# Kernel optimization log

Hardware: AMD Instinct MI355X
Metric: run time of the kernel (lower is better)

The kernel has to match this reference:

```python
import jax, jax.numpy as jnp
import numpy as np

D_MODEL = 1024
QK_DIM = 1024
V_DIM = 1024
H = 16
TAU = 20.0
HQK = QK_DIM // H
HV = V_DIM // H
SCALE = HQK ** -0.5
SCALE_BASE = 512.0
EPS_GAMMA = 1e-8
EPS_GN = 1e-5


def _rotate_every_two(x):
    x1 = x[..., ::2]
    x2 = x[..., 1::2]
    return jnp.stack([-x2, x1], axis=-1).reshape(x.shape)


def _xpos_rotate(q, k, t):
    # q,k: (B,H,N,d); t: (B,N) continuous positions (timestamps in days)
    d = q.shape[-1]
    inv_freq = (1.0 / (10000.0 ** (np.arange(0, d, 2) / d))).astype(np.float32)  # (d/2,)
    sinusoid = t[:, None, :, None] * inv_freq  # (B,1,N,d/2)
    sin = jnp.repeat(jnp.sin(sinusoid), 2, axis=-1)  # (B,1,N,d)
    cos = jnp.repeat(jnp.cos(sinusoid), 2, axis=-1)
    scale_vec = ((np.arange(0, d, 2) + 0.4 * d) / (1.4 * d)).astype(np.float32)  # (d/2,)
    scale = jnp.repeat(scale_vec ** (t[:, None, :, None] / SCALE_BASE), 2, axis=-1)  # (B,1,N,d)
    q_rot = (q * cos + _rotate_every_two(q) * sin) * scale
    k_rot = (k * cos + _rotate_every_two(k) * sin) / scale
    return q_rot, k_rot


def setup_inputs() -> dict:
    key = jax.random.key(0)
    ks = jax.random.split(key, 6)
    B, N = 4, 1024
    X = jax.random.normal(ks[0], (B, N, D_MODEL), dtype=jnp.float32)
    # increasing timestamps in days
    timestamps = jnp.sort(jax.random.uniform(ks[1], (B, N), jnp.float32, 0.0, 100.0), axis=-1)
    W_qkv = jax.random.normal(ks[2], (D_MODEL, 2 * QK_DIM + V_DIM), dtype=jnp.float32) * 0.02
    W_gamma = jax.random.normal(ks[3], (D_MODEL, H), dtype=jnp.float32) * 0.02
    W_gated = jax.random.normal(ks[4], (D_MODEL, V_DIM), dtype=jnp.float32) * 0.02
    W_out = jax.random.normal(ks[5], (V_DIM, D_MODEL), dtype=jnp.float32) * 0.02
    return {"X": X, "timestamps": timestamps, "W_qkv": W_qkv, "W_gamma": W_gamma,
            "W_gated": W_gated, "W_out": W_out}


def reference(X, timestamps, W_qkv, W_gamma, W_gated, W_out):
    B, N, _ = X.shape
    qkv = X @ W_qkv  # (B,N,2*qk+v)
    q, k, v = jnp.split(qkv, [QK_DIM, 2 * QK_DIM], axis=-1)
    q = q.reshape(B, N, H, HQK).transpose(0, 2, 1, 3)  # (B,H,N,dk)
    k = k.reshape(B, N, H, HQK).transpose(0, 2, 1, 3)
    v = v.reshape(B, N, H, HV).transpose(0, 2, 1, 3)
    q, k = _xpos_rotate(q, k, timestamps)
    # data-dependent decay gamma in (0,1]
    gamma = jax.nn.sigmoid(X @ W_gamma) ** (1.0 / TAU)  # (B,N,H)
    log_b = jnp.cumsum(jnp.log(gamma + EPS_GAMMA), axis=1).transpose(0, 2, 1)  # (B,H,N)
    log_D = log_b[..., :, None] - log_b[..., None, :]  # (B,H,N,N)
    causal = jnp.tril(jnp.ones((N, N), dtype=bool))
    # masked_fill(-inf) then clamp[-80,0]: clip maps -inf -> -80 (matches torch)
    D = jnp.exp(jnp.clip(jnp.where(causal, log_D, -jnp.inf), -80.0, 0.0))
    attn = jnp.einsum('bhnd,bhmd->bhnm', q, k) * SCALE * D
    O = jnp.einsum('bhnm,bhmd->bhnd', attn, v)  # (B,H,N,dv)
    O = O.transpose(0, 2, 1, 3).reshape(B, N, V_DIM)
    # GroupNorm(num_groups=H, affine=False) over (channels-in-group, seq)
    g = O.reshape(B, N, H, HV)
    mu = g.mean(axis=(1, 3), keepdims=True)
    var = g.var(axis=(1, 3), keepdims=True)
    O = ((g - mu) / jnp.sqrt(var + EPS_GN)).reshape(B, N, V_DIM)
    O = jax.nn.silu(X @ W_gated) * O
    return O @ W_out
```

## Files before the change

kernel.cpp:

```cpp
#include <hip/hip_runtime.h>
#include <cstddef>
#include <cstdint>

#define NH 16
#define HD 64
#define NSEQ 1024
#define NB 4
#define DM 1024
#define SCALE 0.125f

typedef __attribute__((ext_vector_type(8))) short v8s;
typedef __attribute__((ext_vector_type(4))) float v4f;

__device__ __forceinline__ short f2bf(float x) {
    union { float f; unsigned u; } v; v.f = x;
    unsigned r = v.u + 0x7FFF + ((v.u >> 16) & 1);
    return (short)(r >> 16);
}
__device__ __forceinline__ float bf2f(short x) {
    union { unsigned u; float f; } v; v.u = ((unsigned)(unsigned short)x) << 16;
    return v.f;
}
__device__ __forceinline__ void gload16(const void* g, void* l) {
    __builtin_amdgcn_global_load_lds(
        (const __attribute__((address_space(1))) void*)g,
        (__attribute__((address_space(3))) void*)l, 16, 0, 0);
}
__device__ __forceinline__ int gswz(int r, int kbyte) {
    return (r * 64 + kbyte) ^ (((r >> 1) & 3) << 4);
}
__device__ __forceinline__ int aswz(int r, int byte) {
    return (r * 128 + byte) ^ ((r & 7) << 4);
}
#define SBAR() __builtin_amdgcn_s_barrier()
#define WAITV0() asm volatile("s_waitcnt vmcnt(0)" ::: "memory")
#define WAITV4() asm volatile("s_waitcnt vmcnt(4)" ::: "memory")
#define WAITL() asm volatile("s_waitcnt lgkmcnt(0)" ::: "memory")

__global__ __launch_bounds__(256) void tconv3(const float* __restrict__ Wq,
                                              const float* __restrict__ Wgt,
                                              const float* __restrict__ Wo,
                                              short* __restrict__ Wtq,
                                              short* __restrict__ Wtg,
                                              short* __restrict__ Wto) {
    __shared__ short lsm[32][136];
    int ct = blockIdx.x;
    const int kt = blockIdx.y;
    const float* W; short* Bt; int N;
    if (ct < 24)      { W = Wq;  Bt = Wtq; N = 3072; }
    else if (ct < 32) { W = Wgt; Bt = Wtg; N = 1024; ct -= 24; }
    else              { W = Wo;  Bt = Wto; N = 1024; ct -= 32; }
    const int t = threadIdx.x;
    {
        const int kk = t >> 3, nn0 = (t & 7) * 16;
        const float* src = W + (size_t)(kt * 32 + kk) * N + ct * 128 + nn0;
#pragma unroll
        for (int j = 0; j < 16; j += 4) {
            float4 v = *(const float4*)(src + j);
            lsm[kk][nn0 + j] = f2bf(v.x); lsm[kk][nn0 + j + 1] = f2bf(v.y);
            lsm[kk][nn0 + j + 2] = f2bf(v.z); lsm[kk][nn0 + j + 3] = f2bf(v.w);
        }
    }
    __syncthreads();
    const int rloc = t >> 1, kb0 = (t & 1) * 16;
    short o[16] __attribute__((aligned(16)));
#pragma unroll
    for (int j = 0; j < 16; ++j) o[j] = lsm[kb0 + j][rloc];
    char* base = (char*)(Bt + ((size_t)ct * 32 + kt) * 4096);
#pragma unroll
    for (int c = 0; c < 2; ++c)
        *(v8s*)(base + gswz(rloc, kb0 * 2 + c * 16)) = *(v8s*)&o[c * 8];
}

template<int MODE>
__global__ __launch_bounds__(256) void gemm_tt(const short* __restrict__ A,
                                               const short* __restrict__ B,
                                               void* __restrict__ C, int N,
                                               const short* __restrict__ O,
                                               const float* __restrict__ partial) {
    __shared__ short As[4096];
    __shared__ short Bs[4096];
    const int tid = threadIdx.x;
    const int w = tid >> 6, l = tid & 63;
    const int wr = w >> 1, wc = w & 1;
    const int rt = blockIdx.y, ct = blockIdx.x;
    const char* Abase = (const char*)A + ((size_t)rt * 32) * 8192;
    const char* Bbase = (const char*)B + ((size_t)ct * 32) * 8192;

    v4f acc[4][4];
#pragma unroll
    for (int i = 0; i < 4; ++i)
#pragma unroll
        for (int j = 0; j < 4; ++j) acc[i][j] = (v4f){0.f, 0.f, 0.f, 0.f};

    for (int kt = 0; kt < 32; ++kt) {
        __syncthreads();
#pragma unroll
        for (int i = 0; i < 2; ++i) {
            const int c = w * 2 + i;
            gload16(Abase + (size_t)kt * 8192 + c * 1024 + l * 16, (char*)As + c * 1024);
            gload16(Bbase + (size_t)kt * 8192 + c * 1024 + l * 16, (char*)Bs + c * 1024);
        }
        __syncthreads();
        v8s af[4], bfr[4];
#pragma unroll
        for (int i = 0; i < 4; ++i) {
            const int ra = wr * 64 + i * 16 + (l & 15);
            af[i] = *(const v8s*)((char*)As + gswz(ra, (l >> 4) * 16));
            const int rb = wc * 64 + i * 16 + (l & 15);
            bfr[i] = *(const v8s*)((char*)Bs + gswz(rb, (l >> 4) * 16));
        }
#pragma unroll
        for (int i = 0; i < 4; ++i)
#pragma unroll
            for (int j = 0; j < 4; ++j)
                acc[i][j] = __builtin_amdgcn_mfma_f32_16x16x32_bf16(af[i], bfr[j], acc[i][j], 0, 0, 0);
    }
    float mu = 0.f, rstd = 0.f;
    if (MODE == 2) {
        const int hh = ct * 2 + wc;
        const int bh = (rt >> 3) * NH + hh;
        float s = 0.f, q = 0.f;
#pragma unroll
        for (int i = 0; i < 8; ++i) {
            s += partial[(bh * 8 + i) * 2];
            q += partial[(bh * 8 + i) * 2 + 1];
        }
        const float inv = 1.0f / (NSEQ * HD);
        mu = s * inv;
        rstd = rsqrtf(q * inv - mu * mu + 1e-5f);
    }
#pragma unroll
    for (int i = 0; i < 4; ++i)
#pragma unroll
        for (int j = 0; j < 4; ++j) {
            const int r0 = rt * 128 + wr * 64 + i * 16 + (l >> 4) * 4;
            const int cc = ct * 128 + wc * 64 + j * 16 + (l & 15);
#pragma unroll
            for (int t2 = 0; t2 < 4; ++t2) {
                if (MODE == 1) ((short*)C)[(size_t)(r0 + t2) * N + cc] = f2bf(acc[i][j][t2]);
                else if (MODE == 0) ((float*)C)[(size_t)(r0 + t2) * N + cc] = acc[i][j][t2];
                else {
                    const int row = r0 + t2;
                    const float g = acc[i][j][t2];
                    const float silu = g / (1.0f + __expf(-g));
                    const float ov = bf2f(O[(size_t)row * DM + cc]);
                    const float val = silu * (ov - mu) * rstd;
                    const int rloc = row - rt * 128;
                    char* base = (char*)((short*)C + ((size_t)rt * 32 + (cc >> 5)) * 4096);
                    *(short*)(base + gswz(rloc, (cc & 31) * 2)) = f2bf(val);
                }
            }
        }
}

__global__ __launch_bounds__(256) void gamma_conv(const float* __restrict__ X,
                                                  const float* __restrict__ Wg,
                                                  float* __restrict__ loggam,
                                                  short* __restrict__ Xb) {
    __shared__ float wgs[1024 * 17];
    const int tid = threadIdx.x;
#pragma unroll
    for (int it = 0; it < 16; ++it) {
        const int idx = it * 1024 + tid * 4;
        float4 v = *(const float4*)(Wg + idx);
        const int k = idx >> 4, h0 = idx & 15;
        wgs[k * 17 + h0]     = v.x;
        wgs[k * 17 + h0 + 1] = v.y;
        wgs[k * 17 + h0 + 2] = v.z;
        wgs[k * 17 + h0 + 3] = v.w;
    }
    __syncthreads();

    const int r = tid >> 4, c = tid & 15;
    const int row = blockIdx.x * 16 + r;
    const int rt = row >> 7, rloc = row & 127;
    char* xtile = (char*)(Xb + (size_t)rt * 32 * 4096);
    const float* xrow = X + (size_t)row * DM;
    float acc[16];
#pragma unroll
    for (int h = 0; h < 16; ++h) acc[h] = 0.0f;
#pragma unroll 4
    for (int i = 0; i < 16; ++i) {
        const int kb = i * 64 + c * 4;
        float4 xv = *(const float4*)(xrow + kb);
        short4 o4 = make_short4(f2bf(xv.x), f2bf(xv.y), f2bf(xv.z), f2bf(xv.w));
        *(short4*)(xtile + (size_t)(kb >> 5) * 8192 + gswz(rloc, (kb & 31) * 2)) = o4;
        const float xs[4] = {xv.x, xv.y, xv.z, xv.w};
#pragma unroll
        for (int j = 0; j < 4; ++j) {
            const float* wrow = &wgs[(kb + j) * 17];
#pragma unroll
            for (int h = 0; h < 16; ++h) acc[h] = fmaf(xs[j], wrow[h], acc[h]);
        }
    }
#pragma unroll
    for (int h = 0; h < 16; ++h) {
#pragma unroll
        for (int off = 8; off >= 1; off >>= 1)
            acc[h] += __shfl_xor(acc[h], off, 16);
    }
    const float d = acc[c];
    const float sig = 1.0f / (1.0f + expf(-d));
    const float gam = powf(sig, 1.0f / 20.0f);
    loggam[(size_t)row * NH + c] = logf(gam + 1e-8f);
}

__global__ __launch_bounds__(256) void scan_kernel(const float* __restrict__ lg,
                                                   float* __restrict__ lgT) {
    const int wave = threadIdx.x >> 6;
    const int lane = threadIdx.x & 63;
    const int bh = blockIdx.x * 4 + wave;
    const int b = bh >> 4, h = bh & 15;
    const float* p = lg + (size_t)b * NSEQ * NH + h;
    const int n0 = lane * 16;
    float v[16];
    float s = 0.0f;
#pragma unroll
    for (int j = 0; j < 16; ++j) { v[j] = p[(size_t)(n0 + j) * NH]; s += v[j]; }
    float sc = s;
#pragma unroll
    for (int off = 1; off < 64; off <<= 1) {
        float o = __shfl_up(sc, off, 64);
        if (lane >= off) sc += o;
    }
    float acc = sc - s;
    float* q = lgT + (size_t)bh * NSEQ + n0;
#pragma unroll
    for (int j = 0; j < 16; ++j) { acc += v[j]; q[j] = acc; }
}

__global__ __launch_bounds__(256) void prep(const short* __restrict__ qkvb,
                                            const float* __restrict__ ts,
                                            short* __restrict__ Qb,
                                            short* __restrict__ Kb,
                                            short* __restrict__ Vtb) {
    __shared__ short vsm[64][72];
    const int tile = blockIdx.x, bh = blockIdx.y;
    const int b = bh >> 4, h = bh & 15;
    const int t = threadIdx.x;
    const int rloc = t >> 2, d0 = (t & 3) * 16;
    const int row = b * NSEQ + tile * 64 + rloc;
    const short* src = qkvb + (size_t)row * 3072 + h * HD;
    const size_t tb = ((size_t)bh * 16 + tile) * 4096;

    float qa[16], ka[16];
    {
        v8s q0 = *(const v8s*)(src + d0), q1 = *(const v8s*)(src + d0 + 8);
        v8s k0 = *(const v8s*)(src + 1024 + d0), k1 = *(const v8s*)(src + 1024 + d0 + 8);
#pragma unroll
        for (int j = 0; j < 8; ++j) {
            qa[j] = bf2f(q0[j]); qa[j + 8] = bf2f(q1[j]);
            ka[j] = bf2f(k0[j]); ka[j + 8] = bf2f(k1[j]);
        }
    }
    const float tv = ts[row];
    short qo[16] __attribute__((aligned(16)));
    short ko[16] __attribute__((aligned(16)));
#pragma unroll
    for (int j = 0; j < 8; ++j) {
        const int i = (d0 >> 1) + j;
        const float inv_freq = exp2f(-0.4152410119f * (float)i);
        const float ang = tv * inv_freq;
        const float s = sinf(ang), c = cosf(ang);
        const float sv = ((float)(2 * i) + 25.6f) * (1.0f / 89.6f);
        const float e = log2f(sv) * tv * (1.0f / 512.0f);
        const float sc = exp2f(e) * SCALE, isc = exp2f(-e);
        qo[2 * j]     = f2bf((qa[2 * j] * c - qa[2 * j + 1] * s) * sc);
        qo[2 * j + 1] = f2bf((qa[2 * j + 1] * c + qa[2 * j] * s) * sc);
        ko[2 * j]     = f2bf((ka[2 * j] * c - ka[2 * j + 1] * s) * isc);
        ko[2 * j + 1] = f2bf((ka[2 * j + 1] * c + ka[2 * j] * s) * isc);
    }
#pragma unroll
    for (int c = 0; c < 2; ++c) {
        *(v8s*)((char*)(Qb + tb) + aswz(rloc, d0 * 2 + c * 16)) = *(v8s*)&qo[c * 8];
        *(v8s*)((char*)(Kb + tb) + aswz(rloc, d0 * 2 + c * 16)) = *(v8s*)&ko[c * 8];
    }
    {
        v8s v0 = *(const v8s*)(src + 2048 + d0), v1 = *(const v8s*)(src + 2048 + d0 + 8);
        *(short4*)&vsm[rloc][d0]      = *(short4*)&v0;
        *(short4*)&vsm[rloc][d0 + 4]  = *((short4*)&v0 + 1);
        *(short4*)&vsm[rloc][d0 + 8]  = *(short4*)&v1;
        *(short4*)&vsm[rloc][d0 + 12] = *((short4*)&v1 + 1);
    }
    __syncthreads();
    {
        const int d = t >> 2, m0 = (t & 3) * 16;
        short vt[16] __attribute__((aligned(16)));
#pragma unroll
        for (int j = 0; j < 16; ++j) vt[j] = vsm[m0 + j][d];
#pragma unroll
        for (int c = 0; c < 2; ++c)
            *(v8s*)((char*)(Vtb + tb) + aswz(d, m0 * 2 + c * 16)) = *(v8s*)&vt[c * 8];
    }
}

__global__ __launch_bounds__(256) void attn6(const short* __restrict__ Qb,
                                             const short* __restrict__ Kb,
                                             const short* __restrict__ Vtb,
                                             const float* __restrict__ logbT,
                                             short* __restrict__ O,
                                             float* __restrict__ partial) {
    __shared__ short Ks[2][4096];
    __shared__ short Vts[2][4096];
    __shared__ short Ps[8192];
    __shared__ float lbAll[1024];
    __shared__ float emAll[1024];
    const int id = blockIdx.x;
    const int half = id >> 8;
    const int idx = id & 255;
    const int bh = ((idx & 7) << 3) | ((idx >> 3) & 7);
    const int qq = half == 0 ? (4 + (idx >> 6)) : (3 - (idx >> 6));
    const int b = bh >> 4, h = bh & 15;
    const int tid = threadIdx.x;
    const int w = tid >> 6, l = tid & 63;
    const int n0 = qq * 128;
    const int NT = 2 * qq + 2;

#pragma unroll
    for (int i = 0; i < 4; ++i) {
        const int c = w * 4 + i;
        gload16((const char*)Qb + ((size_t)bh * 16 + 2 * qq) * 8192 + c * 1024 + l * 16,
                (char*)Ps + c * 1024);
    }
    for (int i = tid; i < 1024; i += 256)
        lbAll[i] = logbT[(size_t)bh * NSEQ + i];
    WAITV0(); WAITL();
    SBAR();

    const float base = lbAll[n0];
    for (int i = tid; i < NT * 64; i += 256) emAll[i] = __expf(base - lbAll[i]);
    float en[2];
#pragma unroll
    for (int rg = 0; rg < 2; ++rg)
        en[rg] = __expf(lbAll[n0 + w * 32 + rg * 16 + (l & 15)] - base);
    v8s aq[2][2];
#pragma unroll
    for (int rg = 0; rg < 2; ++rg)
#pragma unroll
        for (int kc = 0; kc < 2; ++kc) {
            const int r = w * 32 + rg * 16 + (l & 15);
            aq[rg][kc] = *(const v8s*)((char*)Ps + (r >> 6) * 8192 +
                                       aswz(r & 63, kc * 64 + (l >> 4) * 16));
        }
    WAITL();
    SBAR();

    v4f oacc[2][4];
#pragma unroll
    for (int rg = 0; rg < 2; ++rg)
#pragma unroll
        for (int dt = 0; dt < 4; ++dt) oacc[rg][dt] = (v4f){0.f, 0.f, 0.f, 0.f};

#pragma unroll
    for (int i = 0; i < 2; ++i) {
        const int c = w * 2 + i;
        gload16((const char*)Kb + ((size_t)bh * 16 + 0) * 8192 + c * 1024 + l * 16,
                (char*)Ks + c * 1024);
        gload16((const char*)Vtb + ((size_t)bh * 16 + 0) * 8192 + c * 1024 + l * 16,
                (char*)Vts + c * 1024);
    }

    for (int t = 0; t < NT; ++t) {
        const int m0 = t * 64;
        const int buf = t & 1;
        SBAR();
        if (t + 1 < NT) {
            const int nb = (t + 1) & 1;
#pragma unroll
            for (int i = 0; i < 2; ++i) {
                const int c = w * 2 + i;
                gload16((const char*)Kb + ((size_t)bh * 16 + t + 1) * 8192 + c * 1024 + l * 16,
                        (char*)Ks + nb * 8192 + c * 1024);
                gload16((const char*)Vtb + ((size_t)bh * 16 + t + 1) * 8192 + c * 1024 + l * 16,
                        (char*)Vts + nb * 8192 + c * 1024);
            }
            WAITV4();
        } else {
            WAITV0();
        }
        SBAR();

        const bool active = (m0 <= n0 + w * 32 + 31);
        if (active) {
            const char* KsB = (const char*)Ks + buf * 8192;
            const char* VtsB = (const char*)Vts + buf * 8192;
            v4f sfr[2][4];
#pragma unroll
            for (int rg = 0; rg < 2; ++rg)
#pragma unroll
                for (int m4 = 0; m4 < 4; ++m4) sfr[rg][m4] = (v4f){0.f, 0.f, 0.f, 0.f};
            __builtin_amdgcn_s_setprio(1);
#pragma unroll
            for (int m4 = 0; m4 < 4; ++m4) {
#pragma unroll
                for (int kc = 0; kc < 2; ++kc) {
                    const int m = m4 * 16 + (l & 15);
                    v8s bk = *(const v8s*)(KsB + aswz(m, kc * 64 + (l >> 4) * 16));
#pragma unroll
                    for (int rg = 0; rg < 2; ++rg)
                        sfr[rg][m4] = __builtin_amdgcn_mfma_f32_16x16x32_bf16(bk, aq[rg][kc], sfr[rg][m4], 0, 0, 0);
                }
            }
            __builtin_amdgcn_s_setprio(0);
            const bool needMask = (m0 + 63) > (n0 + w * 32);
#pragma unroll
            for (int rg = 0; rg < 2; ++rg) {
                const int r = w * 32 + rg * 16 + (l & 15);
                const float enr = en[rg];
#pragma unroll
                for (int m4 = 0; m4 < 4; ++m4) {
                    const int mbase = m0 + m4 * 16 + (l >> 4) * 4;
                    float4 emv = *(const float4*)&emAll[mbase];
                    const float ems[4] = {emv.x, emv.y, emv.z, emv.w};
                    union { short s[4]; uint2 u; } pk;
#pragma unroll
                    for (int t2 = 0; t2 < 4; ++t2) {
                        float sval = sfr[rg][m4][t2] * enr * ems[t2];
                        if (needMask && (n0 + r) < (mbase + t2)) sval = 0.0f;
                        pk.s[t2] = f2bf(sval);
                    }
                    *(uint2*)((char*)Ps + aswz(r, (m4 * 16 + (l >> 4) * 4) * 2)) = pk.u;
                }
            }
            WAITL();
            __builtin_amdgcn_sched_barrier(0);
            __builtin_amdgcn_s_setprio(1);
#pragma unroll
            for (int kc = 0; kc < 2; ++kc) {
                v8s ap[2];
#pragma unroll
                for (int rg = 0; rg < 2; ++rg) {
                    const int r = w * 32 + rg * 16 + (l & 15);
                    ap[rg] = *(const v8s*)((char*)Ps + aswz(r, kc * 64 + (l >> 4) * 16));
                }
#pragma unroll
                for (int dt = 0; dt < 4; ++dt) {
                    const int d = dt * 16 + (l & 15);
                    v8s bv = *(const v8s*)(VtsB + aswz(d, kc * 64 + (l >> 4) * 16));
#pragma unroll
                    for (int rg = 0; rg < 2; ++rg)
                        oacc[rg][dt] = __builtin_amdgcn_mfma_f32_16x16x32_bf16(bv, ap[rg], oacc[rg][dt], 0, 0, 0);
                }
            }
            __builtin_amdgcn_s_setprio(0);
        }
    }
    float psum = 0.0f, pssq = 0.0f;
#pragma unroll
    for (int rg = 0; rg < 2; ++rg) {
        const int row = n0 + w * 32 + rg * 16 + (l & 15);
#pragma unroll
        for (int dt = 0; dt < 4; ++dt) {
            const float a0 = oacc[rg][dt][0], a1 = oacc[rg][dt][1];
            const float a2 = oacc[rg][dt][2], a3 = oacc[rg][dt][3];
            short4 o4 = make_short4(f2bf(a0), f2bf(a1), f2bf(a2), f2bf(a3));
            *(short4*)(O + (size_t)(b * NSEQ + row) * DM + h * HD + dt * 16 + (l >> 4) * 4) = o4;
            psum += a0 + a1 + a2 + a3;
            pssq += a0 * a0 + a1 * a1 + a2 * a2 + a3 * a3;
        }
    }
    __syncthreads();
    float* red = (float*)Ks;
    red[tid] = psum; red[256 + tid] = pssq;
    __syncthreads();
    for (int s = 128; s > 0; s >>= 1) {
        if (tid < s) { red[tid] += red[tid + s]; red[256 + tid] += red[256 + tid + s]; }
        __syncthreads();
    }
    if (tid == 0) {
        partial[(bh * 8 + qq) * 2]     = red[0];
        partial[(bh * 8 + qq) * 2 + 1] = red[256];
    }
}

extern "C" void kernel_launch(void* const* d_in, const int* in_sizes, int n_in,
                              void* d_out, int out_size, void* d_ws, size_t ws_size,
                              hipStream_t stream) {
    const float* X       = (const float*)d_in[0];
    const float* ts      = (const float*)d_in[1];
    const float* W_qkv   = (const float*)d_in[2];
    const float* W_gamma = (const float*)d_in[3];
    const float* W_gated = (const float*)d_in[4];
    const float* W_out   = (const float*)d_in[5];
    float* out = (float*)d_out;

    char* ws = (char*)d_ws;
    short* qkvb = (short*)ws;
    float* logb = (float*)(ws + 25165824);
    short* Oatt = (short*)(ws + 25427968);
    short* Xb   = (short*)(ws + 42205696);
    short* Wtq  = (short*)(ws + 50594304);
    short* Wtg  = (short*)(ws + 56885760);
    short* Wto  = (short*)(ws + 58982912);
    short* Qb   = (short*)(ws + 61080064);
    short* Kb   = (short*)(ws + 69468672);
    short* Vtb  = (short*)(ws + 77857280);
    float* logbT = (float*)(ws + 86245888);
    short* Gb   = Xb;
    float* partial = (float*)Wtq;

    tconv3<<<dim3(40, 32), 256, 0, stream>>>(W_qkv, W_gated, W_out, Wtq, Wtg, Wto);
    gamma_conv<<<256, 256, 0, stream>>>(X, W_gamma, logb, Xb);
    gemm_tt<1><<<dim3(24, 32), 256, 0, stream>>>(Xb, Wtq, qkvb, 3072, nullptr, nullptr);
    scan_kernel<<<16, 256, 0, stream>>>(logb, logbT);
    prep<<<dim3(16, 64), 256, 0, stream>>>(qkvb, ts, Qb, Kb, Vtb);
    attn6<<<512, 256, 0, stream>>>(Qb, Kb, Vtb, logbT, Oatt, partial);
    gemm_tt<2><<<dim3(8, 32), 256, 0, stream>>>(Xb, Wtg, Gb, 1024, Oatt, partial);
    gemm_tt<0><<<dim3(8, 32), 256, 0, stream>>>(Gb, Wto, out, 1024, nullptr, nullptr);
}
```

Baseline: 154.1 us.

## Fuse xPos rotation and V transpose into QKV GEMM epilogue; merge prep kernels

Merges weight conversion, gamma projection/X conversion and a new per-position rotation table (cos, sin, scale, inverse scale) into a single launch. The QKV GEMM epilogue now applies the xPos rotation and scaling directly and writes Q, K and transposed V tiles through LDS. This removes the bf16 qkv intermediate buffer, the separate prep kernel and two launches. The trade-off is a heavier GEMM epilogue with table loads and cross-lane shuffles, and a smaller staging buffer that is reused after the main loop.

```diff
diff --git a/kernel.cpp b/kernel.cpp
--- a/kernel.cpp
+++ b/kernel.cpp
@@ -37,39 +37,207 @@
 #define WAITV4() asm volatile("s_waitcnt vmcnt(4)" ::: "memory")
 #define WAITL() asm volatile("s_waitcnt lgkmcnt(0)" ::: "memory")
 
-__global__ __launch_bounds__(256) void tconv3(const float* __restrict__ Wq,
-                                              const float* __restrict__ Wgt,
-                                              const float* __restrict__ Wo,
-                                              short* __restrict__ Wtq,
-                                              short* __restrict__ Wtg,
-                                              short* __restrict__ Wto) {
-    __shared__ short lsm[32][136];
-    int ct = blockIdx.x;
-    const int kt = blockIdx.y;
-    const float* W; short* Bt; int N;
-    if (ct < 24)      { W = Wq;  Bt = Wtq; N = 3072; }
-    else if (ct < 32) { W = Wgt; Bt = Wtg; N = 1024; ct -= 24; }
-    else              { W = Wo;  Bt = Wto; N = 1024; ct -= 32; }
-    const int t = threadIdx.x;
-    {
-        const int kk = t >> 3, nn0 = (t & 7) * 16;
-        const float* src = W + (size_t)(kt * 32 + kk) * N + ct * 128 + nn0;
-#pragma unroll
-        for (int j = 0; j < 16; j += 4) {
-            float4 v = *(const float4*)(src + j);
-            lsm[kk][nn0 + j] = f2bf(v.x); lsm[kk][nn0 + j + 1] = f2bf(v.y);
-            lsm[kk][nn0 + j + 2] = f2bf(v.z); lsm[kk][nn0 + j + 3] = f2bf(v.w);
-        }
+__global__ __launch_bounds__(256) void prep_inputs(const float* __restrict__ X,
+                                                   const float* __restrict__ ts,
+                                                   const float* __restrict__ Wq,
+                                                   const float* __restrict__ Wg,
+                                                   const float* __restrict__ Wgt,
+                                                   const float* __restrict__ Wo,
+                                                   short* __restrict__ Wtq,
+                                                   short* __restrict__ Wtg,
+                                                   short* __restrict__ Wto,
+                                                   float* __restrict__ loggam,
+                                                   short* __restrict__ Xb,
+                                                   float4* __restrict__ tbl) {
+    __shared__ float smem[1024 * 17];
+    const int bid = blockIdx.x;
+    const int tid = threadIdx.x;
+    if (bid < 1280) {
+        short (*lsm)[136] = (short(*)[136])smem;
+        int ct = bid % 40;
+        const int kt = bid / 40;
+        const float* W; short* Bt; int N;
+        if (ct < 24)      { W = Wq;  Bt = Wtq; N = 3072; }
+        else if (ct < 32) { W = Wgt; Bt = Wtg; N = 1024; ct -= 24; }
+        else              { W = Wo;  Bt = Wto; N = 1024; ct -= 32; }
+        {
+            const int kk = tid >> 3, nn0 = (tid & 7) * 16;
+            const float* src = W + (size_t)(kt * 32 + kk) * N + ct * 128 + nn0;
+#pragma unroll
+            for (int j = 0; j < 16; j += 4) {
+                float4 v = *(const float4*)(src + j);
+                lsm[kk][nn0 + j] = f2bf(v.x); lsm[kk][nn0 + j + 1] = f2bf(v.y);
+                lsm[kk][nn0 + j + 2] = f2bf(v.z); lsm[kk][nn0 + j + 3] = f2bf(v.w);
+            }
+        }
+        __syncthreads();
+        const int rloc = tid >> 1, kb0 = (tid & 1) * 16;
+        short o[16] __attribute__((aligned(16)));
+#pragma unroll
+        for (int j = 0; j < 16; ++j) o[j] = lsm[kb0 + j][rloc];
+        char* base = (char*)(Bt + ((size_t)ct * 32 + kt) * 4096);
+#pragma unroll
+        for (int c = 0; c < 2; ++c)
+            *(v8s*)(base + gswz(rloc, kb0 * 2 + c * 16)) = *(v8s*)&o[c * 8];
+    } else if (bid < 1536) {
+        float* wgs = smem;
+#pragma unroll
+        for (int it = 0; it < 16; ++it) {
+            const int idx = it * 1024 + tid * 4;
+            float4 v = *(const float4*)(Wg + idx);
+            const int k = idx >> 4, h0 = idx & 15;
+            wgs[k * 17 + h0]     = v.x;
+            wgs[k * 17 + h0 + 1] = v.y;
+            wgs[k * 17 + h0 + 2] = v.z;
+            wgs[k * 17 + h0 + 3] = v.w;
+        }
+        __syncthreads();
+        const int r = tid >> 4, c = tid & 15;
+        const int row = (bid - 1280) * 16 + r;
+        const int rt = row >> 7, rloc = row & 127;
+        char* xtile = (char*)(Xb + (size_t)rt * 32 * 4096);
+        const float* xrow = X + (size_t)row * DM;
+        float acc[16];
+#pragma unroll
+        for (int h = 0; h < 16; ++h) acc[h] = 0.0f;
+#pragma unroll 4
+        for (int i = 0; i < 16; ++i) {
+            const int kb = i * 64 + c * 4;
+            float4 xv = *(const float4*)(xrow + kb);
+            short4 o4 = make_short4(f2bf(xv.x), f2bf(xv.y), f2bf(xv.z), f2bf(xv.w));
+            *(short4*)(xtile + (size_t)(kb >> 5) * 8192 + gswz(rloc, (kb & 31) * 2)) = o4;
+            const float xs[4] = {xv.x, xv.y, xv.z, xv.w};
+#pragma unroll
+            for (int j = 0; j < 4; ++j) {
+                const float* wrow = &wgs[(kb + j) * 17];
+#pragma unroll
+                for (int h = 0; h < 16; ++h) acc[h] = fmaf(xs[j], wrow[h], acc[h]);
+            }
+        }
+#pragma unroll
+        for (int h = 0; h < 16; ++h) {
+#pragma unroll
+            for (int off = 8; off >= 1; off >>= 1)
+                acc[h] += __shfl_xor(acc[h], off, 16);
+        }
+        const float d = acc[c];
+        const float sig = 1.0f / (1.0f + expf(-d));
+        const float gam = powf(sig, 1.0f / 20.0f);
+        loggam[(size_t)row * NH + c] = logf(gam + 1e-8f);
+    } else {
+        const int e = (bid - 1536) * 256 + tid;
+        const int row = e >> 5, f = e & 31;
+        const float tv = ts[row];
+        const float inv_freq = exp2f(-0.4152410119f * (float)f);
+        const float ang = tv * inv_freq;
+        const float s = sinf(ang), c = cosf(ang);
+        const float sv = ((float)(2 * f) + 25.6f) * (1.0f / 89.6f);
+        const float ee = log2f(sv) * tv * (1.0f / 512.0f);
+        tbl[e] = make_float4(c, s, exp2f(ee) * SCALE, exp2f(-ee));
+    }
+}
+
+__global__ __launch_bounds__(256) void gemm_qkv(const short* __restrict__ A,
+                                                const short* __restrict__ B,
+                                                const float4* __restrict__ tbl,
+                                                short* __restrict__ Qb,
+                                                short* __restrict__ Kb,
+                                                short* __restrict__ Vtb) {
+    __shared__ short smem[16384];
+    short* As = smem;
+    short* Bs = smem + 4096;
+    const int tid = threadIdx.x;
+    const int w = tid >> 6, l = tid & 63;
+    const int wr = w >> 1, wc = w & 1;
+    const int rt = blockIdx.y, ct = blockIdx.x;
+    const char* Abase = (const char*)A + ((size_t)rt * 32) * 8192;
+    const char* Bbase = (const char*)B + ((size_t)ct * 32) * 8192;
+
+    v4f acc[4][4];
+#pragma unroll
+    for (int i = 0; i < 4; ++i)
+#pragma unroll
+        for (int j = 0; j < 4; ++j) acc[i][j] = (v4f){0.f, 0.f, 0.f, 0.f};
+
+    for (int kt = 0; kt < 32; ++kt) {
+        __syncthreads();
+#pragma unroll
+        for (int i = 0; i < 2; ++i) {
+            const int c = w * 2 + i;
+            gload16(Abase + (size_t)kt * 8192 + c * 1024 + l * 16, (char*)As + c * 1024);
+            gload16(Bbase + (size_t)kt * 8192 + c * 1024 + l * 16, (char*)Bs + c * 1024);
+        }
+        __syncthreads();
+        v8s af[4], bfr[4];
+#pragma unroll
+        for (int i = 0; i < 4; ++i) {
+            const int ra = wr * 64 + i * 16 + (l & 15);
+            af[i] = *(const v8s*)((char*)As + gswz(ra, (l >> 4) * 16));
+            const int rb = wc * 64 + i * 16 + (l & 15);
+            bfr[i] = *(const v8s*)((char*)Bs + gswz(rb, (l >> 4) * 16));
+        }
+#pragma unroll
+        for (int i = 0; i < 4; ++i)
+#pragma unroll
+            for (int j = 0; j < 4; ++j)
+                acc[i][j] = __builtin_amdgcn_mfma_f32_16x16x32_bf16(af[i], bfr[j], acc[i][j], 0, 0, 0);
     }
     __syncthreads();
-    const int rloc = t >> 1, kb0 = (t & 1) * 16;
-    short o[16] __attribute__((aligned(16)));
-#pragma unroll
-    for (int j = 0; j < 16; ++j) o[j] = lsm[kb0 + j][rloc];
-    char* base = (char*)(Bt + ((size_t)ct * 32 + kt) * 4096);
-#pragma unroll
-    for (int c = 0; c < 2; ++c)
-        *(v8s*)(base + gswz(rloc, kb0 * 2 + c * 16)) = *(v8s*)&o[c * 8];
+    char* tbuf = (char*)(smem + w * 4096);
+    const int b = rt >> 3;
+    const int tile = (rt * 2 + wr) & 15;
+
+    if (ct < 16) {
+        const bool isQ = (ct < 8);
+        const int h = isQ ? (2 * ct + wc) : (2 * (ct - 8) + wc);
+        const int fb = (l & 15) >> 1;
+#pragma unroll
+        for (int i = 0; i < 4; ++i) {
+#pragma unroll
+            for (int t2 = 0; t2 < 4; ++t2) {
+                const int rloc64 = i * 16 + (l >> 4) * 4 + t2;
+                const int rglob = rt * 128 + wr * 64 + rloc64;
+#pragma unroll
+                for (int j = 0; j < 4; ++j) {
+                    const float v = acc[i][j][t2];
+                    const float p = __shfl_xor(v, 1);
+                    const float4 T = tbl[rglob * 32 + fb + 8 * j];
+                    const float rot = v * T.x + ((l & 1) ? p * T.y : -(p * T.y));
+                    const float outv = rot * (isQ ? T.z : T.w);
+                    *(short*)(tbuf + aswz(rloc64, (j * 16 + (l & 15)) * 2)) = f2bf(outv);
+                }
+            }
+        }
+        WAITL();
+        __builtin_amdgcn_sched_barrier(0);
+        char* gbase = (char*)((isQ ? Qb : Kb) + ((size_t)(b * 16 + h) * 16 + tile) * 4096);
+#pragma unroll
+        for (int c = 0; c < 8; ++c) {
+            const int off = aswz(l, c * 16);
+            *(v8s*)(gbase + off) = *(const v8s*)(tbuf + off);
+        }
+    } else {
+        const int h = 2 * (ct - 16) + wc;
+#pragma unroll
+        for (int i = 0; i < 4; ++i)
+#pragma unroll
+            for (int j = 0; j < 4; ++j) {
+                const int d = j * 16 + (l & 15);
+                const int m0 = i * 16 + (l >> 4) * 4;
+                union { short s[4]; uint2 u; } pk;
+#pragma unroll
+                for (int t2 = 0; t2 < 4; ++t2) pk.s[t2] = f2bf(acc[i][j][t2]);
+                *(uint2*)(tbuf + aswz(d, m0 * 2)) = pk.u;
+            }
+        WAITL();
+        __builtin_amdgcn_sched_barrier(0);
+        char* gbase = (char*)(Vtb + ((size_t)(b * 16 + h) * 16 + tile) * 4096);
+#pragma unroll
+        for (int c = 0; c < 8; ++c) {
+            const int off = aswz(l, c * 16);
+            *(v8s*)(gbase + off) = *(const v8s*)(tbuf + off);
+        }
+    }
 }
 
 template<int MODE>
@@ -138,8 +306,7 @@
             const int cc = ct * 128 + wc * 64 + j * 16 + (l & 15);
 #pragma unroll
             for (int t2 = 0; t2 < 4; ++t2) {
-                if (MODE == 1) ((short*)C)[(size_t)(r0 + t2) * N + cc] = f2bf(acc[i][j][t2]);
-                else if (MODE == 0) ((float*)C)[(size_t)(r0 + t2) * N + cc] = acc[i][j][t2];
+                if (MODE == 0) ((float*)C)[(size_t)(r0 + t2) * N + cc] = acc[i][j][t2];
                 else {
                     const int row = r0 + t2;
                     const float g = acc[i][j][t2];
@@ -154,58 +321,6 @@
         }
 }
 
-__global__ __launch_bounds__(256) void gamma_conv(const float* __restrict__ X,
-                                                  const float* __restrict__ Wg,
-                                                  float* __restrict__ loggam,
-                                                  short* __restrict__ Xb) {
-    __shared__ float wgs[1024 * 17];
-    const int tid = threadIdx.x;
-#pragma unroll
-    for (int it = 0; it < 16; ++it) {
-        const int idx = it * 1024 + tid * 4;
-        float4 v = *(const float4*)(Wg + idx);
-        const int k = idx >> 4, h0 = idx & 15;
-        wgs[k * 17 + h0]     = v.x;
-        wgs[k * 17 + h0 + 1] = v.y;
-        wgs[k * 17 + h0 + 2] = v.z;
-        wgs[k * 17 + h0 + 3] = v.w;
-    }
-    __syncthreads();
-
-    const int r = tid >> 4, c = tid & 15;
-    const int row = blockIdx.x * 16 + r;
-    const int rt = row >> 7, rloc = row & 127;
-    char* xtile = (char*)(Xb + (size_t)rt * 32 * 4096);
-    const float* xrow = X + (size_t)row * DM;
-    float acc[16];
-#pragma unroll
-    for (int h = 0; h < 16; ++h) acc[h] = 0.0f;
-#pragma unroll 4
-    for (int i = 0; i < 16; ++i) {
-        const int kb = i * 64 + c * 4;
-        float4 xv = *(const float4*)(xrow + kb);
-        short4 o4 = make_short4(f2bf(xv.x), f2bf(xv.y), f2bf(xv.z), f2bf(xv.w));
-        *(short4*)(xtile + (size_t)(kb >> 5) * 8192 + gswz(rloc, (kb & 31) * 2)) = o4;
-        const float xs[4] = {xv.x, xv.y, xv.z, xv.w};
-#pragma unroll
-        for (int j = 0; j < 4; ++j) {
-            const float* wrow = &wgs[(kb + j) * 17];
-#pragma unroll
-            for (int h = 0; h < 16; ++h) acc[h] = fmaf(xs[j], wrow[h], acc[h]);
-        }
-    }
-#pragma unroll
-    for (int h = 0; h < 16; ++h) {
-#pragma unroll
-        for (int off = 8; off >= 1; off >>= 1)
-            acc[h] += __shfl_xor(acc[h], off, 16);
-    }
-    const float d = acc[c];
-    const float sig = 1.0f / (1.0f + expf(-d));
-    const float gam = powf(sig, 1.0f / 20.0f);
-    loggam[(size_t)row * NH + c] = logf(gam + 1e-8f);
-}
-
 __global__ __launch_bounds__(256) void scan_kernel(const float* __restrict__ lg,
                                                    float* __restrict__ lgT) {
     const int wave = threadIdx.x >> 6;
@@ -228,71 +343,6 @@
     float* q = lgT + (size_t)bh * NSEQ + n0;
 #pragma unroll
     for (int j = 0; j < 16; ++j) { acc += v[j]; q[j] = acc; }
-}
-
-__global__ __launch_bounds__(256) void prep(const short* __restrict__ qkvb,
-                                            const float* __restrict__ ts,
-                                            short* __restrict__ Qb,
-                                            short* __restrict__ Kb,
-                                            short* __restrict__ Vtb) {
-    __shared__ short vsm[64][72];
-    const int tile = blockIdx.x, bh = blockIdx.y;
-    const int b = bh >> 4, h = bh & 15;
-    const int t = threadIdx.x;
-    const int rloc = t >> 2, d0 = (t & 3) * 16;
-    const int row = b * NSEQ + tile * 64 + rloc;
-    const short* src = qkvb + (size_t)row * 3072 + h * HD;
-    const size_t tb = ((size_t)bh * 16 + tile) * 4096;
-
-    float qa[16], ka[16];
-    {
-        v8s q0 = *(const v8s*)(src + d0), q1 = *(const v8s*)(src + d0 + 8);
-        v8s k0 = *(const v8s*)(src + 1024 + d0), k1 = *(const v8s*)(src + 1024 + d0 + 8);
-#pragma unroll
-        for (int j = 0; j < 8; ++j) {
-            qa[j] = bf2f(q0[j]); qa[j + 8] = bf2f(q1[j]);
-            ka[j] = bf2f(k0[j]); ka[j + 8] = bf2f(k1[j]);
-        }
-    }
-    const float tv = ts[row];
-    short qo[16] __attribute__((aligned(16)));
-    short ko[16] __attribute__((aligned(16)));
-#pragma unroll
-    for (int j = 0; j < 8; ++j) {
-        const int i = (d0 >> 1) + j;
-        const float inv_freq = exp2f(-0.4152410119f * (float)i);
-        const float ang = tv * inv_freq;
-        const float s = sinf(ang), c = cosf(ang);
-        const float sv = ((float)(2 * i) + 25.6f) * (1.0f / 89.6f);
-        const float e = log2f(sv) * tv * (1.0f / 512.0f);
-        const float sc = exp2f(e) * SCALE, isc = exp2f(-e);
-        qo[2 * j]     = f2bf((qa[2 * j] * c - qa[2 * j + 1] * s) * sc);
-        qo[2 * j + 1] = f2bf((qa[2 * j + 1] * c + qa[2 * j] * s) * sc);
-        ko[2 * j]     = f2bf((ka[2 * j] * c - ka[2 * j + 1] * s) * isc);
-        ko[2 * j + 1] = f2bf((ka[2 * j + 1] * c + ka[2 * j] * s) * isc);
-    }
-#pragma unroll
-    for (int c = 0; c < 2; ++c) {
-        *(v8s*)((char*)(Qb + tb) + aswz(rloc, d0 * 2 + c * 16)) = *(v8s*)&qo[c * 8];
-        *(v8s*)((char*)(Kb + tb) + aswz(rloc, d0 * 2 + c * 16)) = *(v8s*)&ko[c * 8];
-    }
-    {
-        v8s v0 = *(const v8s*)(src + 2048 + d0), v1 = *(const v8s*)(src + 2048 + d0 + 8);
-        *(short4*)&vsm[rloc][d0]      = *(short4*)&v0;
-        *(short4*)&vsm[rloc][d0 + 4]  = *((short4*)&v0 + 1);
-        *(short4*)&vsm[rloc][d0 + 8]  = *(short4*)&v1;
-        *(short4*)&vsm[rloc][d0 + 12] = *((short4*)&v1 + 1);
-    }
-    __syncthreads();
-    {
-        const int d = t >> 2, m0 = (t & 3) * 16;
-        short vt[16] __attribute__((aligned(16)));
-#pragma unroll
-        for (int j = 0; j < 16; ++j) vt[j] = vsm[m0 + j][d];
-#pragma unroll
-        for (int c = 0; c < 2; ++c)
-            *(v8s*)((char*)(Vtb + tb) + aswz(d, m0 * 2 + c * 16)) = *(v8s*)&vt[c * 8];
-    }
 }
 
 __global__ __launch_bounds__(256) void attn6(const short* __restrict__ Qb,
@@ -486,25 +536,24 @@
     float* out = (float*)d_out;
 
     char* ws = (char*)d_ws;
-    short* qkvb = (short*)ws;
-    float* logb = (float*)(ws + 25165824);
-    short* Oatt = (short*)(ws + 25427968);
-    short* Xb   = (short*)(ws + 42205696);
-    short* Wtq  = (short*)(ws + 50594304);
-    short* Wtg  = (short*)(ws + 56885760);
-    short* Wto  = (short*)(ws + 58982912);
-    short* Qb   = (short*)(ws + 61080064);
-    short* Kb   = (short*)(ws + 69468672);
-    short* Vtb  = (short*)(ws + 77857280);
-    float* logbT = (float*)(ws + 86245888);
-    short* Gb   = Xb;
-    float* partial = (float*)Wtq;
-
-    tconv3<<<dim3(40, 32), 256, 0, stream>>>(W_qkv, W_gated, W_out, Wtq, Wtg, Wto);
-    gamma_conv<<<256, 256, 0, stream>>>(X, W_gamma, logb, Xb);
-    gemm_tt<1><<<dim3(24, 32), 256, 0, stream>>>(Xb, Wtq, qkvb, 3072, nullptr, nullptr);
+    short*  Xb    = (short*)(ws + 0);
+    short*  Wtq   = (short*)(ws + 8388608);
+    short*  Wtg   = (short*)(ws + 14680064);
+    short*  Wto   = (short*)(ws + 16777216);
+    short*  Qb    = (short*)(ws + 18874368);
+    short*  Kb    = (short*)(ws + 27262976);
+    short*  Vtb   = (short*)(ws + 35651584);
+    float*  logb  = (float*)(ws + 44040192);
+    float*  logbT = (float*)(ws + 44302336);
+    float4* tbl   = (float4*)(ws + 44564480);
+    short*  Oatt  = (short*)(ws + 46661632);
+    float*  partial = (float*)(ws + 55050240);
+    short*  Gb    = (short*)(ws + 55054336);
+
+    prep_inputs<<<2048, 256, 0, stream>>>(X, ts, W_qkv, W_gamma, W_gated, W_out,
+                                          Wtq, Wtg, Wto, logb, Xb, tbl);
     scan_kernel<<<16, 256, 0, stream>>>(logb, logbT);
-    prep<<<dim3(16, 64), 256, 0, stream>>>(qkvb, ts, Qb, Kb, Vtb);
+    gemm_qkv<<<dim3(24, 32), 256, 0, stream>>>(Xb, Wtq, tbl, Qb, Kb, Vtb);
     attn6<<<512, 256, 0, stream>>>(Qb, Kb, Vtb, logbT, Oatt, partial);
     gemm_tt<2><<<dim3(8, 32), 256, 0, stream>>>(Xb, Wtg, Gb, 1024, Oatt, partial);
     gemm_tt<0><<<dim3(8, 32), 256, 0, stream>>>(Gb, Wto, out, 1024, nullptr, nullptr);
```

Measured after the change: 162.2 us. 1.05x slower.
